# Kernel optimization log

Hardware: AMD Instinct MI355X
Metric: run time of the kernel (lower is better)

## Reference

```python
import jax, jax.numpy as jnp
import numpy as np

B, C_IN, C_OUT = 2, 32, 32
N_IN = 128 * 128            # input grid points
N_OUT = 128 * 128           # output grid points
KERNEL_SIZE = 9             # (3-1)*4 + 1 for kernel_shape=[3,4], piecewise_linear basis
NNZ = 1_500_000             # sparse entries in psi (kernel_size, n_out, n_in)


def setup_inputs() -> dict:
    key = jax.random.key(0)
    ks = jax.random.split(key, 8)
    scale = (1.0 / C_IN) ** 0.5  # sqrt(1/groupsize), groups=1
    return {
        "x": jax.random.normal(ks[0], (B, C_IN, N_IN), jnp.float32),
        "quadrature_weights": jax.random.uniform(ks[1], (N_IN,), jnp.float32, 0.5, 1.5) / N_IN,
        "psi_vals": jax.random.uniform(ks[2], (NNZ,), jnp.float32),
        "weight": scale * jax.random.normal(ks[3], (C_OUT, C_IN, KERNEL_SIZE), jnp.float32),
        "bias": jnp.zeros((C_OUT,), jnp.float32),
        "psi_idx_k": jax.random.randint(ks[4], (NNZ,), 0, KERNEL_SIZE, dtype=jnp.int32),
        "psi_idx_out": jax.random.randint(ks[5], (NNZ,), 0, N_OUT, dtype=jnp.int32),
        "psi_idx_in": jax.random.randint(ks[6], (NNZ,), 0, N_IN, dtype=jnp.int32),
        "n_out": N_OUT,
    }


def reference(x, quadrature_weights, psi_vals, weight, bias,
              psi_idx_k, psi_idx_out, psi_idx_in, n_out):
    # x: (B, C, n_in); weight: (O, C, K); psi is sparse (K, n_out, n_in)
    Bb, C, n_in = x.shape
    K = weight.shape[2]
    # pre-multiply by quadrature weights, layout (n_in, B, C) for gather
    xq = (x * quadrature_weights[None, None, :]).transpose(2, 0, 1)
    # gather-weight: contribution of each sparse entry  -> (nnz, B, C)
    contrib = xq[psi_idx_in] * psi_vals[:, None, None]
    # scatter-add into (kernel, out) bins == sparse psi @ xq
    seg = psi_idx_k * n_out + psi_idx_out
    xk = jax.ops.segment_sum(contrib, seg, num_segments=K * n_out)
    xk = xk.reshape(K, n_out, Bb, C)  # (K, n_out, B, C)
    # channel/kernel mixing with learned weight (groups=1)
    out = jnp.einsum("knbc,ock->bon", xk, weight) + bias[None, :, None]
    return out  # (B, out_channels, n_out)
```

## Files before the change

### kernel.cpp

```cpp
#include <hip/hip_runtime.h>

#define N_IN   16384
#define N_OUT  16384
#define KSZ    9
#define CIN    32
#define COUT   32
#define BC     64
#define NCB    1024
#define CHA    4096
#define ECAP_F 2048
#define GSTR   16
#define ROWS   144
#define XSTR   68

union PrepSH {
    struct { int cnt[NCB]; int cntE[NCB]; int gbase[NCB]; int cursor[NCB];
             int segsum[8]; float2 slist[CHA]; } bin;
    struct { float tile[64 * 65]; } xqp;
};

__global__ __launch_bounds__(512) void k_prep(
        const float* __restrict__ x, const float* __restrict__ qw,
        const float* __restrict__ vals, const float* __restrict__ w,
        const int* __restrict__ ik, const int* __restrict__ io,
        const int* __restrict__ ii, float* __restrict__ xq,
        float2* __restrict__ sivF, int* __restrict__ gcntF,
        float* __restrict__ wT, int nnz, int nchA) {
    __shared__ PrepSH sh;
    const int t = threadIdx.x;
    const int bid = blockIdx.x;

    if (bid >= nchA) {
        if (bid < nchA + 256) {
            const int in0 = (bid - nchA) * 64;
#pragma unroll
            for (int i = 0; i < 8; ++i) {
                int idx = t + i * 512;
                int bcl = idx >> 6, inl = idx & 63;
                sh.xqp.tile[bcl * 65 + inl] = x[bcl * N_IN + in0 + inl];
            }
            __syncthreads();
#pragma unroll
            for (int i = 0; i < 8; ++i) {
                int idx = t + i * 512;
                int inl = idx >> 6, bcl = idx & 63;
                xq[(size_t)(in0 + inl) * BC + bcl] = sh.xqp.tile[bcl * 65 + inl] * qw[in0 + inl];
            }
        } else {
            for (int i = t; i < COUT * CIN * KSZ; i += 512) {
                int o = i / (CIN * KSZ);
                int r = i - o * (CIN * KSZ);
                int c = r / KSZ;
                int k = r - c * KSZ;
                wT[((k * 8 + (o >> 2)) * 32 + c) * 4 + (o & 3)] = w[i];
            }
        }
        return;
    }

    sh.bin.cnt[t] = 0;
    sh.bin.cnt[t + 512] = 0;
    __syncthreads();
    const int base = bid * CHA;
    const int e0   = base + t * 8;

    float vv[8]; int pk[8]; int bk[8]; bool hv[8];
    if (e0 + 8 <= nnz) {
        int4 a0 = *(const int4*)(io + e0),  a1 = *(const int4*)(io + e0 + 4);
        int4 b0 = *(const int4*)(ii + e0),  b1 = *(const int4*)(ii + e0 + 4);
        int4 k0 = *(const int4*)(ik + e0),  k1 = *(const int4*)(ik + e0 + 4);
        float4 d0 = *(const float4*)(vals + e0), d1 = *(const float4*)(vals + e0 + 4);
        int ov[8] = {a0.x, a0.y, a0.z, a0.w, a1.x, a1.y, a1.z, a1.w};
        int iv[8] = {b0.x, b0.y, b0.z, b0.w, b1.x, b1.y, b1.z, b1.w};
        int kv[8] = {k0.x, k0.y, k0.z, k0.w, k1.x, k1.y, k1.z, k1.w};
        float dv[8] = {d0.x, d0.y, d0.z, d0.w, d1.x, d1.y, d1.z, d1.w};
#pragma unroll
        for (int j = 0; j < 8; ++j) {
            hv[j] = true;
            bk[j] = ov[j] >> 4;
            pk[j] = (int)(((unsigned)(ov[j] >> 4) << 22)) | (iv[j] << 8) | (kv[j] * 16 + (ov[j] & 15));
            vv[j] = dv[j];
        }
    } else {
#pragma unroll
        for (int j = 0; j < 8; ++j) {
            int e = e0 + j;
            hv[j] = (e < nnz);
            if (hv[j]) {
                int o = io[e];
                bk[j] = o >> 4;
                pk[j] = (int)(((unsigned)(o >> 4) << 22)) | (ii[e] << 8) | (ik[e] * 16 + (o & 15));
                vv[j] = vals[e];
            } else { bk[j] = 0; pk[j] = 0; vv[j] = 0.f; }
        }
    }
#pragma unroll
    for (int j = 0; j < 8; ++j) if (hv[j]) atomicAdd(&sh.bin.cnt[bk[j]], 1);
    __syncthreads();

    const int lane = t & 63;
    const int wvp  = t >> 6;
    int cvv[2], exclv[2];
    {
        int carry = 0;
#pragma unroll
        for (int s = 0; s < 2; ++s) {
            const int idx = wvp * 128 + s * 64 + lane;
            const int cv = sh.bin.cnt[idx];
            cvv[s] = cv;
            sh.bin.gbase[idx] = idx * ECAP_F + (cv ? atomicAdd(&gcntF[idx * GSTR], cv) : 0);
            int v = cv;
#pragma unroll
            for (int off = 1; off < 64; off <<= 1) {
                int u = __shfl_up(v, off);
                if (lane >= off) v += u;
            }
            exclv[s] = carry + v - cv;
            carry += __shfl(v, 63);
        }
        if (lane == 0) sh.bin.segsum[wvp] = carry;
    }
    __syncthreads();
    if (t == 0) {
        int c = 0;
#pragma unroll
        for (int s = 0; s < 8; ++s) { int xs = sh.bin.segsum[s]; sh.bin.segsum[s] = c; c += xs; }
    }
    __syncthreads();
#pragma unroll
    for (int s = 0; s < 2; ++s) {
        const int idx = wvp * 128 + s * 64 + lane;
        const int e = exclv[s] + sh.bin.segsum[wvp];
        sh.bin.cntE[idx]   = e;
        sh.bin.cursor[idx] = e;
    }
    __syncthreads();
#pragma unroll
    for (int j = 0; j < 8; ++j) {
        if (hv[j]) {
            int pos = atomicAdd(&sh.bin.cursor[bk[j]], 1);
            sh.bin.slist[pos] = make_float2(vv[j], __int_as_float(pk[j]));
        }
    }
    __syncthreads();
    const int m = min(nnz - base, CHA);
    for (int p = t; p < m; p += 512) {
        float2 f2 = sh.bin.slist[p];
        int cb = (int)((unsigned)__float_as_int(f2.y) >> 22);
        int dest = sh.bin.gbase[cb] + (p - sh.bin.cntE[cb]);
        if (dest < (cb + 1) * ECAP_F) sivF[dest] = f2;
    }
}

__global__ __launch_bounds__(512) void k_fused8(const float* __restrict__ xq,
        const float2* __restrict__ sivF, const int* __restrict__ gcntF,
        const float* __restrict__ wT, const float* __restrict__ bias,
        float* __restrict__ out) {
    __shared__ __align__(16) float sxk[80 * XSTR];
    __shared__ __align__(16) float2 slist[ECAP_F];
    __shared__ int    rowStart[ROWS + 1];
    __shared__ int    cursor[ROWS];
    const int tid  = threadIdx.x;
    const int lane = tid & 63;
    const int wv   = __builtin_amdgcn_readfirstlane(tid >> 6);
    const unsigned f = blockIdx.x;

    if (tid < ROWS) rowStart[tid] = 0;
    __syncthreads();

    const int mF = min(gcntF[f * GSTR], ECAP_F);
    const float2* __restrict__ src = sivF + (size_t)f * ECAP_F;
    const int* __restrict__ srcI = (const int*)src;
    for (int i = tid; i < mF; i += 512)
        atomicAdd(&rowStart[srcI[2 * i + 1] & 0xFF], 1);
    __syncthreads();

    if (wv == 0) {
        int carry = 0;
#pragma unroll
        for (int i0 = 0; i0 < 192; i0 += 64) {
            int idx = i0 + lane;
            int v = (idx < ROWS) ? rowStart[idx] : 0;
            int orig = v;
#pragma unroll
            for (int off = 1; off < 64; off <<= 1) {
                int u = __shfl_up(v, off);
                if (lane >= off) v += u;
            }
            if (idx < ROWS) {
                int excl = carry + v - orig;
                rowStart[idx] = excl;
                cursor[idx]   = excl;
            }
            carry += __shfl(v, 63);
        }
        if (lane == 0) rowStart[ROWS] = carry;
    }
    __syncthreads();
    for (int i = tid; i < mF; i += 512) {
        float2 v = src[i];
        int p = __float_as_int(v.y);
        int pos = atomicAdd(&cursor[p & 0xFF], 1);
        slist[pos] = make_float2(v.x, __int_as_float(p & 0x3FFF00));
    }
    __syncthreads();

    const char* xqb   = (const char*)xq;
    const int   lane4 = lane * 4;
    const int   h     = lane >> 4;
    const int   nl    = lane & 15;
    float acc[4] = {0.f, 0.f, 0.f, 0.f};

#pragma unroll
    for (int ph = 0; ph < 2; ++ph) {
        const int rbase = ph ? 80 : 0;
        const int rend  = ph ? 144 : 80;
        const int nrows = rend - rbase;
        for (int i = tid; i < nrows * XSTR; i += 512) sxk[i] = 0.f;
        __syncthreads();
        for (int r = rbase + wv; r < rend; r += 8) {
            const int a = rowStart[r], b = rowStart[r + 1];
            if (a >= b) continue;
            float acc0 = 0.f, acc1 = 0.f, acc2 = 0.f, acc3 = 0.f;
            int i = a;
            for (; i + 7 < b; i += 8) {
                float2 v0 = slist[i],     v1 = slist[i + 1], v2 = slist[i + 2], v3 = slist[i + 3];
                float2 v4 = slist[i + 4], v5 = slist[i + 5], v6 = slist[i + 6], v7 = slist[i + 7];
                acc0 += *(const float*)(xqb + (__float_as_int(v0.y) + lane4)) * v0.x;
                acc1 += *(const float*)(xqb + (__float_as_int(v1.y) + lane4)) * v1.x;
                acc2 += *(const float*)(xqb + (__float_as_int(v2.y) + lane4)) * v2.x;
                acc3 += *(const float*)(xqb + (__float_as_int(v3.y) + lane4)) * v3.x;
                acc0 += *(const float*)(xqb + (__float_as_int(v4.y) + lane4)) * v4.x;
                acc1 += *(const float*)(xqb + (__float_as_int(v5.y) + lane4)) * v5.x;
                acc2 += *(const float*)(xqb + (__float_as_int(v6.y) + lane4)) * v6.x;
                acc3 += *(const float*)(xqb + (__float_as_int(v7.y) + lane4)) * v7.x;
            }
            for (; i + 3 < b; i += 4) {
                float2 v0 = slist[i], v1 = slist[i + 1], v2 = slist[i + 2], v3 = slist[i + 3];
                acc0 += *(const float*)(xqb + (__float_as_int(v0.y) + lane4)) * v0.x;
                acc1 += *(const float*)(xqb + (__float_as_int(v1.y) + lane4)) * v1.x;
                acc2 += *(const float*)(xqb + (__float_as_int(v2.y) + lane4)) * v2.x;
                acc3 += *(const float*)(xqb + (__float_as_int(v3.y) + lane4)) * v3.x;
            }
            for (; i < b; ++i) {
                float2 v = slist[i];
                acc0 += *(const float*)(xqb + (__float_as_int(v.y) + lane4)) * v.x;
            }
            sxk[(r - rbase) * XSTR + lane] = (acc0 + acc1) + (acc2 + acc3);
        }
        __syncthreads();
        if (lane < 32) {
            const int kbase = ph ? 5 : 0;
            const int kcnt  = ph ? 4 : 5;
            for (int kk = 0; kk < kcnt; ++kk) {
                const float* xr = &sxk[(kk * 16 + nl) * XSTR + h * 32];
                const float* wp = &wT[((kbase + kk) * 8 + wv) * 128];
#pragma unroll
                for (int c4 = 0; c4 < 8; ++c4) {
                    float4 xv = *(const float4*)&xr[c4 * 4];
#pragma unroll
                    for (int cc = 0; cc < 4; ++cc) {
                        float xval = (&xv.x)[cc];
#pragma unroll
                        for (int j = 0; j < 4; ++j)
                            acc[j] += xval * wp[(c4 * 4 + cc) * 4 + j];
                    }
                }
            }
        }
        __syncthreads();
    }

    if (lane < 32) {
        const int n0 = (int)f * 16;
#pragma unroll
        for (int j = 0; j < 4; ++j) {
            int o = wv * 4 + j;
            out[((size_t)h * COUT + o) * N_OUT + n0 + nl] = acc[j] + bias[o];
        }
    }
}

extern "C" void kernel_launch(void* const* d_in, const int* in_sizes, int n_in,
                              void* d_out, int out_size, void* d_ws, size_t ws_size,
                              hipStream_t stream) {
    const float* x    = (const float*)d_in[0];
    const float* qw   = (const float*)d_in[1];
    const float* vals = (const float*)d_in[2];
    const float* w    = (const float*)d_in[3];
    const float* bias = (const float*)d_in[4];
    const int*   ik   = (const int*)d_in[5];
    const int*   io   = (const int*)d_in[6];
    const int*   ii   = (const int*)d_in[7];
    const int    nnz  = in_sizes[2];
    const int    nchA = (nnz + CHA - 1) / CHA;

    char* ws = (char*)d_ws;
    float*  xq    = (float*)ws;  ws += (size_t)N_IN * BC * 4;
    float2* sivF  = (float2*)ws; ws += (size_t)NCB * ECAP_F * 8;
    int*    gcntF = (int*)ws;    ws += (size_t)NCB * GSTR * 4;
    float*  wT    = (float*)ws;  ws += (size_t)COUT * CIN * KSZ * 4;

    hipMemsetAsync(gcntF, 0, (size_t)NCB * GSTR * sizeof(int), stream);
    k_prep  <<<nchA + 257, 512, 0, stream>>>(x, qw, vals, w, ik, io, ii,
                                             xq, sivF, gcntF, wT, nnz, nchA);
    k_fused8<<<NCB, 512, 0, stream>>>(xq, sivF, gcntF, wT, bias, (float*)d_out);
}
```

Before: 174.0 us.

## Scatter entries directly to global bins and stage bin list in shared memory

The prep kernel no longer sorts each chunk in shared memory before writing. It counts per-bin entries, reserves global space with one atomic per bin, then re-reads the input and scatters each entry straight to its global slot through a shared-memory atomic cursor. Chunk size doubles and block size halves, which cuts shared-memory use and removes the scans and extra barriers, but global writes become uncoalesced and the index array is read twice. The fused kernel now copies each bin's entries into shared memory on the first pass, so the second pass reads shared memory instead of global.

```diff
diff --git a/kernel.cpp b/kernel.cpp
--- a/kernel.cpp
+++ b/kernel.cpp
@@ -7,19 +7,18 @@
 #define COUT   32
 #define BC     64
 #define NCB    1024
-#define CHA    4096
+#define CHA    8192
 #define ECAP_F 2048
 #define GSTR   16
 #define ROWS   144
 #define XSTR   68
 
 union PrepSH {
-    struct { int cnt[NCB]; int cntE[NCB]; int gbase[NCB]; int cursor[NCB];
-             int segsum[8]; float2 slist[CHA]; } bin;
-    struct { float tile[64 * 65]; } xqp;
+    int   cnt[NCB];
+    float tile[64 * 65];
 };
 
-__global__ __launch_bounds__(512) void k_prep(
+__global__ __launch_bounds__(256) void k_prep2(
         const float* __restrict__ x, const float* __restrict__ qw,
         const float* __restrict__ vals, const float* __restrict__ w,
         const int* __restrict__ ik, const int* __restrict__ io,
@@ -34,20 +33,20 @@
         if (bid < nchA + 256) {
             const int in0 = (bid - nchA) * 64;
 #pragma unroll
-            for (int i = 0; i < 8; ++i) {
-                int idx = t + i * 512;
+            for (int i = 0; i < 16; ++i) {
+                int idx = t + i * 256;
                 int bcl = idx >> 6, inl = idx & 63;
-                sh.xqp.tile[bcl * 65 + inl] = x[bcl * N_IN + in0 + inl];
+                sh.tile[bcl * 65 + inl] = x[bcl * N_IN + in0 + inl];
             }
             __syncthreads();
 #pragma unroll
-            for (int i = 0; i < 8; ++i) {
-                int idx = t + i * 512;
+            for (int i = 0; i < 16; ++i) {
+                int idx = t + i * 256;
                 int inl = idx >> 6, bcl = idx & 63;
-                xq[(size_t)(in0 + inl) * BC + bcl] = sh.xqp.tile[bcl * 65 + inl] * qw[in0 + inl];
+                xq[(size_t)(in0 + inl) * BC + bcl] = sh.tile[bcl * 65 + inl] * qw[in0 + inl];
             }
         } else {
-            for (int i = t; i < COUT * CIN * KSZ; i += 512) {
+            for (int i = t; i < COUT * CIN * KSZ; i += 256) {
                 int o = i / (CIN * KSZ);
                 int r = i - o * (CIN * KSZ);
                 int c = r / KSZ;
@@ -58,101 +57,67 @@
         return;
     }
 
-    sh.bin.cnt[t] = 0;
-    sh.bin.cnt[t + 512] = 0;
+    for (int i = t; i < NCB; i += 256) sh.cnt[i] = 0;
     __syncthreads();
     const int base = bid * CHA;
-    const int e0   = base + t * 8;
-
-    float vv[8]; int pk[8]; int bk[8]; bool hv[8];
-    if (e0 + 8 <= nnz) {
-        int4 a0 = *(const int4*)(io + e0),  a1 = *(const int4*)(io + e0 + 4);
-        int4 b0 = *(const int4*)(ii + e0),  b1 = *(const int4*)(ii + e0 + 4);
-        int4 k0 = *(const int4*)(ik + e0),  k1 = *(const int4*)(ik + e0 + 4);
-        float4 d0 = *(const float4*)(vals + e0), d1 = *(const float4*)(vals + e0 + 4);
-        int ov[8] = {a0.x, a0.y, a0.z, a0.w, a1.x, a1.y, a1.z, a1.w};
-        int iv[8] = {b0.x, b0.y, b0.z, b0.w, b1.x, b1.y, b1.z, b1.w};
-        int kv[8] = {k0.x, k0.y, k0.z, k0.w, k1.x, k1.y, k1.z, k1.w};
-        float dv[8] = {d0.x, d0.y, d0.z, d0.w, d1.x, d1.y, d1.z, d1.w};
+    const bool full = (base + CHA <= nnz);
+
+    if (full) {
 #pragma unroll
         for (int j = 0; j < 8; ++j) {
-            hv[j] = true;
-            bk[j] = ov[j] >> 4;
-            pk[j] = (int)(((unsigned)(ov[j] >> 4) << 22)) | (iv[j] << 8) | (kv[j] * 16 + (ov[j] & 15));
-            vv[j] = dv[j];
+            int4 o4 = *(const int4*)(io + base + (t + j * 256) * 4);
+            atomicAdd(&sh.cnt[o4.x >> 4], 1);
+            atomicAdd(&sh.cnt[o4.y >> 4], 1);
+            atomicAdd(&sh.cnt[o4.z >> 4], 1);
+            atomicAdd(&sh.cnt[o4.w >> 4], 1);
         }
     } else {
+        const int iN = nnz - base;
+        for (int i = t; i < iN; i += 256)
+            atomicAdd(&sh.cnt[io[base + i] >> 4], 1);
+    }
+    __syncthreads();
+
+    for (int i = t; i < NCB; i += 256) {
+        int cv = sh.cnt[i];
+        sh.cnt[i] = i * ECAP_F + (cv ? atomicAdd(&gcntF[i * GSTR], cv) : 0);
+    }
+    __syncthreads();
+
+    if (full) {
 #pragma unroll
         for (int j = 0; j < 8; ++j) {
-            int e = e0 + j;
-            hv[j] = (e < nnz);
-            if (hv[j]) {
-                int o = io[e];
-                bk[j] = o >> 4;
-                pk[j] = (int)(((unsigned)(o >> 4) << 22)) | (ii[e] << 8) | (ik[e] * 16 + (o & 15));
-                vv[j] = vals[e];
-            } else { bk[j] = 0; pk[j] = 0; vv[j] = 0.f; }
-        }
-    }
-#pragma unroll
-    for (int j = 0; j < 8; ++j) if (hv[j]) atomicAdd(&sh.bin.cnt[bk[j]], 1);
-    __syncthreads();
-
-    const int lane = t & 63;
-    const int wvp  = t >> 6;
-    int cvv[2], exclv[2];
-    {
-        int carry = 0;
-#pragma unroll
-        for (int s = 0; s < 2; ++s) {
-            const int idx = wvp * 128 + s * 64 + lane;
-            const int cv = sh.bin.cnt[idx];
-            cvv[s] = cv;
-            sh.bin.gbase[idx] = idx * ECAP_F + (cv ? atomicAdd(&gcntF[idx * GSTR], cv) : 0);
-            int v = cv;
-#pragma unroll
-            for (int off = 1; off < 64; off <<= 1) {
-                int u = __shfl_up(v, off);
-                if (lane >= off) v += u;
-            }
-            exclv[s] = carry + v - cv;
-            carry += __shfl(v, 63);
-        }
-        if (lane == 0) sh.bin.segsum[wvp] = carry;
-    }
-    __syncthreads();
-    if (t == 0) {
-        int c = 0;
-#pragma unroll
-        for (int s = 0; s < 8; ++s) { int xs = sh.bin.segsum[s]; sh.bin.segsum[s] = c; c += xs; }
-    }
-    __syncthreads();
-#pragma unroll
-    for (int s = 0; s < 2; ++s) {
-        const int idx = wvp * 128 + s * 64 + lane;
-        const int e = exclv[s] + sh.bin.segsum[wvp];
-        sh.bin.cntE[idx]   = e;
-        sh.bin.cursor[idx] = e;
-    }
-    __syncthreads();
-#pragma unroll
-    for (int j = 0; j < 8; ++j) {
-        if (hv[j]) {
-            int pos = atomicAdd(&sh.bin.cursor[bk[j]], 1);
-            sh.bin.slist[pos] = make_float2(vv[j], __int_as_float(pk[j]));
-        }
-    }
-    __syncthreads();
-    const int m = min(nnz - base, CHA);
-    for (int p = t; p < m; p += 512) {
-        float2 f2 = sh.bin.slist[p];
-        int cb = (int)((unsigned)__float_as_int(f2.y) >> 22);
-        int dest = sh.bin.gbase[cb] + (p - sh.bin.cntE[cb]);
-        if (dest < (cb + 1) * ECAP_F) sivF[dest] = f2;
+            const int e = base + (t + j * 256) * 4;
+            int4   o4 = *(const int4*)(io + e);
+            int4   i4 = *(const int4*)(ii + e);
+            int4   k4 = *(const int4*)(ik + e);
+            float4 d4 = *(const float4*)(vals + e);
+            int ov[4] = {o4.x, o4.y, o4.z, o4.w};
+            int iv[4] = {i4.x, i4.y, i4.z, i4.w};
+            int kv[4] = {k4.x, k4.y, k4.z, k4.w};
+            float dv[4] = {d4.x, d4.y, d4.z, d4.w};
+#pragma unroll
+            for (int u = 0; u < 4; ++u) {
+                int bk = ov[u] >> 4;
+                int pk = (int)(((unsigned)bk << 22)) | (iv[u] << 8) | (kv[u] * 16 + (ov[u] & 15));
+                int pos = atomicAdd(&sh.cnt[bk], 1);
+                if (pos < (bk + 1) * ECAP_F) sivF[pos] = make_float2(dv[u], __int_as_float(pk));
+            }
+        }
+    } else {
+        const int iN = nnz - base;
+        for (int i = t; i < iN; i += 256) {
+            int e = base + i;
+            int o = io[e];
+            int bk = o >> 4;
+            int pk = (int)(((unsigned)bk << 22)) | (ii[e] << 8) | (ik[e] * 16 + (o & 15));
+            int pos = atomicAdd(&sh.cnt[bk], 1);
+            if (pos < (bk + 1) * ECAP_F) sivF[pos] = make_float2(vals[e], __int_as_float(pk));
+        }
     }
 }
 
-__global__ __launch_bounds__(512) void k_fused8(const float* __restrict__ xq,
+__global__ __launch_bounds__(512) void k_fused9(const float* __restrict__ xq,
         const float2* __restrict__ sivF, const int* __restrict__ gcntF,
         const float* __restrict__ wT, const float* __restrict__ bias,
         float* __restrict__ out) {
@@ -170,9 +135,13 @@
 
     const int mF = min(gcntF[f * GSTR], ECAP_F);
     const float2* __restrict__ src = sivF + (size_t)f * ECAP_F;
-    const int* __restrict__ srcI = (const int*)src;
-    for (int i = tid; i < mF; i += 512)
-        atomicAdd(&rowStart[srcI[2 * i + 1] & 0xFF], 1);
+    float2* tmp = (float2*)sxk;
+
+    for (int i = tid; i < mF; i += 512) {
+        float2 v = src[i];
+        tmp[i] = v;
+        atomicAdd(&rowStart[__float_as_int(v.y) & 0xFF], 1);
+    }
     __syncthreads();
 
     if (wv == 0) {
@@ -198,7 +167,7 @@
     }
     __syncthreads();
     for (int i = tid; i < mF; i += 512) {
-        float2 v = src[i];
+        float2 v = tmp[i];
         int p = __float_as_int(v.y);
         int pos = atomicAdd(&cursor[p & 0xFF], 1);
         slist[pos] = make_float2(v.x, __int_as_float(p & 0x3FFF00));
@@ -302,7 +271,7 @@
     float*  wT    = (float*)ws;  ws += (size_t)COUT * CIN * KSZ * 4;
 
     hipMemsetAsync(gcntF, 0, (size_t)NCB * GSTR * sizeof(int), stream);
-    k_prep  <<<nchA + 257, 512, 0, stream>>>(x, qw, vals, w, ik, io, ii,
+    k_prep2 <<<nchA + 257, 256, 0, stream>>>(x, qw, vals, w, ik, io, ii,
                                              xq, sivF, gcntF, wT, nnz, nchA);
-    k_fused8<<<NCB, 512, 0, stream>>>(xq, sivF, gcntF, wT, bias, (float*)d_out);
+    k_fused9<<<NCB, 512, 0, stream>>>(xq, sivF, gcntF, wT, bias, (float*)d_out);
 }
```

Result: slower. 179.7 us (+3.2%).
